# Kernel optimization log

Measured on AMD Instinct MI355X. Metric: run time of the kernel, lower is better.

## Reference

```python
import jax, jax.numpy as jnp
import numpy as np

F0 = 39          # FIELD_COUNT
D = 16           # embedding dim
SIZES = [128, 128, 128]  # cross_layer_sizes
B = 8192


def setup_inputs() -> dict:
    key = jax.random.key(0)
    k0, k1, k2, k3, k4 = jax.random.split(key, 5)
    nn_input = jax.random.normal(k0, (B, F0 * D), dtype=jnp.float32)
    # direct=False => field_nums: [39, 64, 64]; filters: [F0*Fk, L]
    scale = 0.02
    f0 = jax.random.normal(k1, (F0 * F0, SIZES[0]), dtype=jnp.float32) * scale
    f1 = jax.random.normal(k2, (F0 * (SIZES[0] // 2), SIZES[1]), dtype=jnp.float32) * scale
    f2 = jax.random.normal(k3, (F0 * (SIZES[1] // 2), SIZES[2]), dtype=jnp.float32) * scale
    final_len = SIZES[0] // 2 + SIZES[1] // 2 + SIZES[2]  # 256
    w_nn = jax.random.normal(k4, (final_len, 1), dtype=jnp.float32) * scale
    b_nn = jnp.zeros((1,), dtype=jnp.float32)
    return {"nn_input": nn_input, "f0": f0, "f1": f1, "f2": f2,
            "w_nn": w_nn, "b_nn": b_nn}


def reference(nn_input, f0, f1, f2, w_nn, b_nn):
    x0 = nn_input.reshape(-1, F0, D)            # [B, F0, D]
    b = x0.shape[0]
    filters = [f0, f1, f2]
    hidden = x0
    field = F0
    direct_outs = []
    n_layers = len(SIZES)
    for idx, layer_size in enumerate(SIZES):
        # dim-wise outer product: z[b,d,i*field+j] = x0[b,i,d]*hidden[b,j,d]
        z = jnp.einsum('bid,bjd->bdij', x0, hidden).reshape(b, D, F0 * field)
        if idx == 0:
            # remove self-interactions: keep strictly upper triangle, x2
            mask = jnp.triu(jnp.ones((F0, F0), dtype=z.dtype), k=1).reshape(1, 1, F0 * F0)
            z = z * mask * 2.0
        # conv1d kernel-width-1 == per-position GEMM; fuse the [0,2,1] transpose
        curr = jnp.einsum('bdc,cl->bld', z, filters[idx])   # [B, L, D]
        curr = jax.nn.relu(curr)                            # cross_activation='relu'
        if idx != n_layers - 1:
            half = layer_size // 2
            next_hidden = curr[:, :half, :]
            direct = curr[:, half:, :]
        else:
            direct = curr
            next_hidden = None
        direct_outs.append(direct)
        hidden = next_hidden
        field = layer_size // 2
    result = jnp.concatenate(direct_outs, axis=1)   # [B, final_len, D]
    rs = result.sum(axis=-1)                        # [B, final_len]
    base_score = rs.sum(axis=1, keepdims=True)      # res=True
    return base_score + rs @ w_nn + b_nn            # [B, 1]
```

## Files before the change

### kernel.cpp

```cpp
#include <hip/hip_runtime.h>


#define F0N 39
#define NB  32
#define NC16 156
#define LAYER_HALVES (NC16 * 4 * 64 * 8)
#define IHALFS 8192

typedef _Float16 half8 __attribute__((ext_vector_type(8)));
typedef float f32x16 __attribute__((ext_vector_type(16)));

__global__ void prep_kernel(const float* __restrict__ f0,
                            const float* __restrict__ f1,
                            const float* __restrict__ f2,
                            _Float16* __restrict__ fprep) {
    int blk  = blockIdx.x;
    int l    = blk / NC16;
    int c16  = blk - l * NC16;
    int t    = threadIdx.x;
    int nt   = t >> 6;
    int lane = t & 63;
    int hf   = lane >> 5;
    int n    = nt * 32 + (lane & 31);
    const float* f = (l == 0) ? f0 : ((l == 1) ? f1 : f2);
    half8 v;
    #pragma unroll
    for (int reg = 0; reg < 8; ++reg) {
        int kg = c16 * 16 + hf * 8 + reg;
        float x;
        if (l == 0) {
            int fi = kg >> 6, fj = kg & 63;
            x = (fj < F0N && fj > fi) ? 2.0f * f[(fi * F0N + fj) * 128 + n] : 0.0f;
        } else {
            x = f[(size_t)kg * 128 + n];
        }
        v[reg] = (_Float16)x;
    }
    *(half8*)&fprep[(size_t)l * LAYER_HALVES + (((c16 * 4 + nt) * 64 + lane) << 3)] = v;
}

#define FULL_STEP_LS(Q)                                                       \
    do {                                                                      \
        half8 Bf[4];                                                          \
        _Pragma("unroll")                                                     \
        for (int nt = 0; nt < 4; ++nt)                                        \
            Bf[nt] = *(const half8*)&bcur[(((Q) * 4 + nt) * 64 + lane) << 3]; \
        half8 Af[2];                                                          \
        _Pragma("unroll")                                                     \
        for (int mt = 0; mt < 2; ++mt) Af[mt] = hreg[mt][(Q)] * xv2[mt];      \
        _Pragma("unroll")                                                     \
        for (int mt = 0; mt < 2; ++mt)                                        \
            _Pragma("unroll")                                                 \
            for (int nt = 0; nt < 4; ++nt)                                    \
                acc[mt][nt] = __builtin_amdgcn_mfma_f32_32x32x16_f16(         \
                    Af[mt], Bf[nt], acc[mt][nt], 0, 0, 0);                    \
    } while (0)

#define STAGE_LOAD(IP)                                                        \
    do {                                                                      \
        const uint4* g = (const uint4*)(fpl + (size_t)(IP) * IHALFS);         \
        s0 = g[t];                                                            \
        s1 = g[t + 512];                                                      \
    } while (0)

#define STAGE_WRITE(BUFP)                                                     \
    do {                                                                      \
        ((uint4*)(BUFP))[t]       = s0;                                       \
        ((uint4*)(BUFP))[t + 512] = s1;                                       \
    } while (0)

__global__ __launch_bounds__(512, 2) void cin_mfma(
    const float* __restrict__ xin,
    const _Float16* __restrict__ fprep,
    const float* __restrict__ wnn,
    const float* __restrict__ bnn,
    float* __restrict__ out)
{
    __shared__ _Float16 hT[NB * 16 * 72] __attribute__((aligned(16)));
    __shared__ _Float16 xs[NB * 16 * 40] __attribute__((aligned(16)));
    __shared__ _Float16 bst[2][IHALFS] __attribute__((aligned(16)));
    __shared__ float outacc[NB];

    const int t     = threadIdx.x;
    const int wave  = t >> 6;
    const int lane  = t & 63;
    const int hf    = lane >> 5;
    const int lane5 = lane & 31;
    const int dl    = lane & 15;
    const int bt    = lane5 >> 4;
    const int wb0   = wave * 4;
    const int b0    = blockIdx.x * NB;

    for (int u = t; u < NB * 16 * 72 / 8; u += 512) ((uint4*)hT)[u] = uint4{0, 0, 0, 0};
    if (t < NB) outacc[t] = 0.0f;
    __syncthreads();

    for (int u = t; u < NB * F0N; u += 512) {
        int nb = u / F0N;
        int i  = u - nb * F0N;
        const float* src = xin + (size_t)(b0 + nb) * 624 + i * 16;
        #pragma unroll
        for (int q = 0; q < 4; ++q) {
            float4 v = *(const float4*)(src + q * 4);
            int d = q * 4;
            hT[(nb * 16 + d + 0) * 72 + i] = (_Float16)v.x;
            hT[(nb * 16 + d + 1) * 72 + i] = (_Float16)v.y;
            hT[(nb * 16 + d + 2) * 72 + i] = (_Float16)v.z;
            hT[(nb * 16 + d + 3) * 72 + i] = (_Float16)v.w;
            xs[(nb * 16 + d + 0) * 40 + i] = (_Float16)v.x;
            xs[(nb * 16 + d + 1) * 40 + i] = (_Float16)v.y;
            xs[(nb * 16 + d + 2) * 40 + i] = (_Float16)v.z;
            xs[(nb * 16 + d + 3) * 40 + i] = (_Float16)v.w;
        }
    }
    __syncthreads();

    for (int layer = 0; layer < 3; ++layer) {
        const _Float16* fpl = fprep + (size_t)layer * LAYER_HALVES;
        uint4 s0, s1;

        STAGE_LOAD(0);

        half8 hreg[2][4];
        #pragma unroll
        for (int mt = 0; mt < 2; ++mt) {
            int base = ((wb0 + mt * 2 + bt) * 16 + dl) * 72 + hf * 8;
            #pragma unroll
            for (int r = 0; r < 4; ++r)
                hreg[mt][r] = *(const half8*)&hT[base + r * 16];
        }
        __syncthreads();

        STAGE_WRITE(bst[0]);
        __syncthreads();

        f32x16 acc[2][4];
        #pragma unroll
        for (int mt = 0; mt < 2; ++mt)
            #pragma unroll
            for (int nt = 0; nt < 4; ++nt)
                #pragma unroll
                for (int e = 0; e < 16; ++e) acc[mt][nt][e] = 0.0f;

        const int xrow0 = ((wb0 + bt) * 16 + dl) * 40;
        const int xrow1 = ((wb0 + 2 + bt) * 16 + dl) * 40;

        if (layer == 0) {
            _Float16 xv2[2];
            for (int i = 0; i < 38; ++i) {
                const _Float16* bcur = bst[i & 1];
                _Float16* bnxt = bst[(i & 1) ^ 1];
                if (i < 37) STAGE_LOAD(i + 1);
                xv2[0] = xs[xrow0 + i];
                xv2[1] = xs[xrow1 + i];
                if (i < 15) FULL_STEP_LS(0);
                if (i < 31) FULL_STEP_LS(1);
                if (i < 37) STAGE_WRITE(bnxt);
                FULL_STEP_LS(2);
                __syncthreads();
            }
        } else {
            _Float16 xv2[2];
            for (int i = 0; i < F0N; ++i) {
                const _Float16* bcur = bst[i & 1];
                _Float16* bnxt = bst[(i & 1) ^ 1];
                if (i < F0N - 1) STAGE_LOAD(i + 1);
                xv2[0] = xs[xrow0 + i];
                xv2[1] = xs[xrow1 + i];
                FULL_STEP_LS(0);
                FULL_STEP_LS(1);
                FULL_STEP_LS(2);
                if (i < F0N - 1) STAGE_WRITE(bnxt);
                FULL_STEP_LS(3);
                __syncthreads();
            }
        }

        const int catbase = (layer == 2) ? 128 : ((layer == 0) ? -64 : 0);
        #pragma unroll
        for (int mt = 0; mt < 2; ++mt) {
            const int nb0 = wb0 + mt * 2;
            float cm0 = 0.0f, cm1 = 0.0f;
            #pragma unroll
            for (int nt = 0; nt < 4; ++nt) {
                float r[16];
                #pragma unroll
                for (int reg = 0; reg < 16; ++reg)
                    r[reg] = fmaxf(acc[mt][nt][reg], 0.0f);
                if (layer < 2 && nt < 2) {
                    const int j = nt * 32 + lane5;
                    #pragma unroll
                    for (int reg = 0; reg < 16; ++reg) {
                        int nb = nb0 + (reg >> 3);
                        int d  = (reg & 3) + 8 * ((reg >> 2) & 1) + 4 * hf;
                        hT[(nb * 16 + d) * 72 + j] = (_Float16)r[reg];
                    }
                }
                if (layer == 2 || nt >= 2) {
                    const float w = 1.0f + wnn[catbase + nt * 32 + lane5];
                    float s0r = ((r[0] + r[1]) + (r[2] + r[3])) +
                                ((r[4] + r[5]) + (r[6] + r[7]));
                    float s1r = ((r[8] + r[9]) + (r[10] + r[11])) +
                                ((r[12] + r[13]) + (r[14] + r[15]));
                    s0r += __shfl_xor(s0r, 32, 64);
                    s1r += __shfl_xor(s1r, 32, 64);
                    cm0 = fmaf(s0r, w, cm0);
                    cm1 = fmaf(s1r, w, cm1);
                }
            }
            #pragma unroll
            for (int sh = 16; sh >= 1; sh >>= 1) {
                cm0 += __shfl_xor(cm0, sh, 64);
                cm1 += __shfl_xor(cm1, sh, 64);
            }
            if (lane == 0) {
                atomicAdd(&outacc[nb0], cm0);
                atomicAdd(&outacc[nb0 + 1], cm1);
            }
        }
        __syncthreads();
    }

    if (t < NB) out[b0 + t] = outacc[t] + bnn[0];
}

extern "C" void kernel_launch(void* const* d_in, const int* in_sizes, int n_in,
                              void* d_out, int out_size, void* d_ws, size_t ws_size,
                              hipStream_t stream) {
    const float* xin = (const float*)d_in[0];
    const float* f0g = (const float*)d_in[1];
    const float* f1g = (const float*)d_in[2];
    const float* f2g = (const float*)d_in[3];
    const float* wnn = (const float*)d_in[4];
    const float* bnn = (const float*)d_in[5];
    float* out = (float*)d_out;
    _Float16* fprep = (_Float16*)d_ws;

    prep_kernel<<<3 * NC16, 256, 0, stream>>>(f0g, f1g, f2g, fprep);

    const int B = in_sizes[0] / 624;
    cin_mfma<<<B / NB, 512, 0, stream>>>(xin, fprep, wnn, bnn, out);
}
```

Before: 238.1 us.

## Re-tile waves to 4 M-tiles x 2 N-tiles to halve B fragment LDS loads

```diff
diff --git a/kernel.cpp b/kernel.cpp
--- a/kernel.cpp
+++ b/kernel.cpp
@@ -41,19 +41,17 @@
 
 #define FULL_STEP_LS(Q)                                                       \
     do {                                                                      \
-        half8 Bf[4];                                                          \
+        const _Float16* bq = &bcur[((((Q) * 4 + nh2) * 64) + lane) << 3];     \
+        half8 Bf0 = *(const half8*)bq;                                        \
+        half8 Bf1 = *(const half8*)(bq + 512);                                \
         _Pragma("unroll")                                                     \
-        for (int nt = 0; nt < 4; ++nt)                                        \
-            Bf[nt] = *(const half8*)&bcur[(((Q) * 4 + nt) * 64 + lane) << 3]; \
-        half8 Af[2];                                                          \
-        _Pragma("unroll")                                                     \
-        for (int mt = 0; mt < 2; ++mt) Af[mt] = hreg[mt][(Q)] * xv2[mt];      \
-        _Pragma("unroll")                                                     \
-        for (int mt = 0; mt < 2; ++mt)                                        \
-            _Pragma("unroll")                                                 \
-            for (int nt = 0; nt < 4; ++nt)                                    \
-                acc[mt][nt] = __builtin_amdgcn_mfma_f32_32x32x16_f16(         \
-                    Af[mt], Bf[nt], acc[mt][nt], 0, 0, 0);                    \
+        for (int mt = 0; mt < 4; ++mt) {                                      \
+            half8 Af = hreg[mt][(Q)] * xv2[mt];                               \
+            acc[mt][0] = __builtin_amdgcn_mfma_f32_32x32x16_f16(              \
+                Af, Bf0, acc[mt][0], 0, 0, 0);                                \
+            acc[mt][1] = __builtin_amdgcn_mfma_f32_32x32x16_f16(              \
+                Af, Bf1, acc[mt][1], 0, 0, 0);                                \
+        }                                                                     \
     } while (0)
 
 #define STAGE_LOAD(IP)                                                        \
@@ -88,7 +86,8 @@
     const int lane5 = lane & 31;
     const int dl    = lane & 15;
     const int bt    = lane5 >> 4;
-    const int wb0   = wave * 4;
+    const int bg    = wave >> 1;
+    const int nh2   = (wave & 1) * 2;
     const int b0    = blockIdx.x * NB;
 
     for (int u = t; u < NB * 16 * 72 / 8; u += 512) ((uint4*)hT)[u] = uint4{0, 0, 0, 0};
@@ -121,10 +120,10 @@
 
         STAGE_LOAD(0);
 
-        half8 hreg[2][4];
-        #pragma unroll
-        for (int mt = 0; mt < 2; ++mt) {
-            int base = ((wb0 + mt * 2 + bt) * 16 + dl) * 72 + hf * 8;
+        half8 hreg[4][4];
+        #pragma unroll
+        for (int mt = 0; mt < 4; ++mt) {
+            int base = ((bg * 8 + mt * 2 + bt) * 16 + dl) * 72 + hf * 8;
             #pragma unroll
             for (int r = 0; r < 4; ++r)
                 hreg[mt][r] = *(const half8*)&hT[base + r * 16];
@@ -134,25 +133,27 @@
         STAGE_WRITE(bst[0]);
         __syncthreads();
 
-        f32x16 acc[2][4];
-        #pragma unroll
-        for (int mt = 0; mt < 2; ++mt)
-            #pragma unroll
-            for (int nt = 0; nt < 4; ++nt)
+        f32x16 acc[4][2];
+        #pragma unroll
+        for (int mt = 0; mt < 4; ++mt)
+            #pragma unroll
+            for (int nt = 0; nt < 2; ++nt)
                 #pragma unroll
                 for (int e = 0; e < 16; ++e) acc[mt][nt][e] = 0.0f;
 
-        const int xrow0 = ((wb0 + bt) * 16 + dl) * 40;
-        const int xrow1 = ((wb0 + 2 + bt) * 16 + dl) * 40;
+        int xrow[4];
+        #pragma unroll
+        for (int mt = 0; mt < 4; ++mt)
+            xrow[mt] = ((bg * 8 + mt * 2 + bt) * 16 + dl) * 40;
 
         if (layer == 0) {
-            _Float16 xv2[2];
+            _Float16 xv2[4];
             for (int i = 0; i < 38; ++i) {
                 const _Float16* bcur = bst[i & 1];
                 _Float16* bnxt = bst[(i & 1) ^ 1];
                 if (i < 37) STAGE_LOAD(i + 1);
-                xv2[0] = xs[xrow0 + i];
-                xv2[1] = xs[xrow1 + i];
+                #pragma unroll
+                for (int mt = 0; mt < 4; ++mt) xv2[mt] = xs[xrow[mt] + i];
                 if (i < 15) FULL_STEP_LS(0);
                 if (i < 31) FULL_STEP_LS(1);
                 if (i < 37) STAGE_WRITE(bnxt);
@@ -160,13 +161,13 @@
                 __syncthreads();
             }
         } else {
-            _Float16 xv2[2];
+            _Float16 xv2[4];
             for (int i = 0; i < F0N; ++i) {
                 const _Float16* bcur = bst[i & 1];
                 _Float16* bnxt = bst[(i & 1) ^ 1];
                 if (i < F0N - 1) STAGE_LOAD(i + 1);
-                xv2[0] = xs[xrow0 + i];
-                xv2[1] = xs[xrow1 + i];
+                #pragma unroll
+                for (int mt = 0; mt < 4; ++mt) xv2[mt] = xs[xrow[mt] + i];
                 FULL_STEP_LS(0);
                 FULL_STEP_LS(1);
                 FULL_STEP_LS(2);
@@ -178,17 +179,18 @@
 
         const int catbase = (layer == 2) ? 128 : ((layer == 0) ? -64 : 0);
         #pragma unroll
-        for (int mt = 0; mt < 2; ++mt) {
-            const int nb0 = wb0 + mt * 2;
+        for (int mt = 0; mt < 4; ++mt) {
+            const int nb0 = bg * 8 + mt * 2;
             float cm0 = 0.0f, cm1 = 0.0f;
             #pragma unroll
-            for (int nt = 0; nt < 4; ++nt) {
+            for (int nt = 0; nt < 2; ++nt) {
+                const int gnt = nh2 + nt;
                 float r[16];
                 #pragma unroll
                 for (int reg = 0; reg < 16; ++reg)
                     r[reg] = fmaxf(acc[mt][nt][reg], 0.0f);
-                if (layer < 2 && nt < 2) {
-                    const int j = nt * 32 + lane5;
+                if (layer < 2 && gnt < 2) {
+                    const int j = gnt * 32 + lane5;
                     #pragma unroll
                     for (int reg = 0; reg < 16; ++reg) {
                         int nb = nb0 + (reg >> 3);
@@ -196,8 +198,8 @@
                         hT[(nb * 16 + d) * 72 + j] = (_Float16)r[reg];
                     }
                 }
-                if (layer == 2 || nt >= 2) {
-                    const float w = 1.0f + wnn[catbase + nt * 32 + lane5];
+                if (layer == 2 || gnt >= 2) {
+                    const float w = 1.0f + wnn[catbase + gnt * 32 + lane5];
                     float s0r = ((r[0] + r[1]) + (r[2] + r[3])) +
                                 ((r[4] + r[5]) + (r[6] + r[7]));
                     float s1r = ((r[8] + r[9]) + (r[10] + r[11])) +
@@ -213,7 +215,7 @@
                 cm0 += __shfl_xor(cm0, sh, 64);
                 cm1 += __shfl_xor(cm1, sh, 64);
             }
-            if (lane == 0) {
+            if (lane == 0 && (nh2 == 2 || layer == 2)) {
                 atomicAdd(&outacc[nb0], cm0);
                 atomicAdd(&outacc[nb0 + 1], cm1);
             }
```

After: 262.8 us. 10.4% more time.
